# Optimization experiments

Measured on AMD Instinct MI355X. Metric: run time of the kernel, lower is better.

## Reference

```python
import jax, jax.numpy as jnp
import numpy as np


def _dwconv3x3(x, w, b):
    # depthwise 3x3, stride 1, padding 1 (groups == channels)
    y = jax.lax.conv_general_dilated(
        x, w, window_strides=(1, 1), padding=((1, 1), (1, 1)),
        dimension_numbers=('NCHW', 'OIHW', 'NCHW'),
        feature_group_count=x.shape[1])
    return y + b[None, :, None, None]


def _maxpool(x, f):
    # adaptive_max_pool2d to (h//f, w//f) with h,w divisible by f == stride-f max pool
    return jax.lax.reduce_window(x, -jnp.inf, jax.lax.max,
                                 (1, 1, f, f), (1, 1, f, f), 'VALID')


def _up_nearest(x, f):
    return jnp.repeat(jnp.repeat(x, f, axis=2), f, axis=3)


def setup_inputs() -> dict:
    key = jax.random.key(0)
    ks = jax.random.split(key, 10)
    B, C, H, W = 4, 32, 128, 128
    x = jax.random.normal(ks[0], (B, C, H, W), dtype=jnp.float32)
    mk = lambda k, shape, s: jax.random.normal(k, shape, dtype=jnp.float32) * s
    return {
        'x': x,
        'w0': mk(ks[1], (C, 1, 3, 3), 0.3), 'b0': mk(ks[2], (C,), 0.05),
        'w1': mk(ks[3], (C, 1, 3, 3), 0.3), 'b1': mk(ks[4], (C,), 0.05),
        'w2': mk(ks[5], (C, 1, 3, 3), 0.3), 'b2': mk(ks[6], (C,), 0.05),
        'wa': mk(ks[7], (C, C, 1, 1), 0.2), 'ba': mk(ks[8], (C,), 0.05),
    }


def reference(x, w0, b0, w1, b1, w2, b2, wa, ba):
    b, c, h, w = x.shape
    # multi-scale depthwise feature refinement
    s0 = _dwconv3x3(x, w0, b0)                               # level 0: full res
    s1 = _up_nearest(_dwconv3x3(_maxpool(x, 2), w1, b1), 2)  # level 1: /2
    s2 = _up_nearest(_dwconv3x3(_maxpool(x, 4), w2, b2), 4)  # level 2: /4
    # Channel_mixing8: q=s0, k=s1, v=s2; per-pixel CxC outer product
    to_nc = lambda t: t.transpose(0, 2, 3, 1).reshape(-1, c)  # (N, C), N=b*h*w
    q, k, v = to_nc(s0), to_nc(s1), to_nc(s2)
    kv = v[:, :, None] * k[:, None, :]        # (N, C, C) = v_embed @ k_embed^T
    attn = jax.nn.softmax(kv, axis=1)         # softmax over dim=1 (v axis)
    qkv = jnp.einsum('nij,nj->ni', attn, q)   # matvec with q
    out = qkv.reshape(b, h, w, c).transpose(0, 3, 1, 2)
    # aggr: 1x1 conv; drop_path=0 -> identity
    out = jnp.einsum('bchw,oc->bohw', out, wa[:, :, 0, 0]) + ba[None, :, None, None]
    return jax.nn.gelu(out, approximate=False) * x
```

## Files before the change

kernel.cpp:

```cpp
#include <hip/hip_runtime.h>
#include <hip/hip_fp16.h>
#include <math.h>


__device__ __forceinline__ float2 h2f2(unsigned int u) {
  __half2 h = *reinterpret_cast<__half2*>(&u);
  return __half22float2(h);
}
__device__ __forceinline__ unsigned int f2h2(float a, float b) {
  __half2 h = __floats2half2_rn(a, b);
  return *reinterpret_cast<unsigned int*>(&h);
}

__global__ __launch_bounds__(256) void fused_safm(
    const float* __restrict__ x,
    const float* __restrict__ w0, const float* __restrict__ b0,
    const float* __restrict__ w1, const float* __restrict__ b1,
    const float* __restrict__ w2, const float* __restrict__ b2,
    const float* __restrict__ wa, const float* __restrict__ ba,
    float* __restrict__ out) {
  int bid = blockIdx.x;
  int tw = bid & 7, th = (bid >> 3) & 63, b = bid >> 9;
  int t = threadIdx.x;
  int h4 = th >> 1;

  __shared__ __align__(16) unsigned int regA[4128];
  __shared__ __align__(16) float s0s[1056];
  __shared__ __align__(16) float vsh[288];
  __shared__ __align__(16) float qkvs[1056];
  __shared__ __align__(16) float rds[264];
  float* p1s = (float*)regA;

  {
#pragma unroll
    for (int kk = 0; kk < 9; ++kk) {
      int idx = t + kk * 256;
      int c = idx / 72, rem = idx % 72;
      int r = rem / 12, w = rem % 12;
      int pr = 2 * h4 - 2 + r, pc = 8 * tw - 2 + w;
      float v = 0.f;
      if ((unsigned)pr < 64u && (unsigned)pc < 64u) {
        const float* xp = x + ((size_t)(b * 32 + c) << 14) + 2 * pr * 128 + 2 * pc;
        float2 r0 = *(const float2*)xp;
        float2 r1 = *(const float2*)(xp + 128);
        v = fmaxf(fmaxf(r0.x, r0.y), fmaxf(r1.x, r1.y));
      }
      p1s[c * 73 + r * 12 + w] = v;
    }
  }
  {
    int c = t >> 3, gg = t & 7;
    int hh = gg >> 2, wb = (gg & 3) * 4;
    const float* xp = x + ((size_t)(b * 32 + c) << 14);
    const float* wc = w0 + c * 9;
    float wv[9];
#pragma unroll
    for (int q = 0; q < 9; ++q) wv[q] = wc[q];
    float bz = b0[c];
    float a0 = bz, a1 = bz, a2 = bz, a3 = bz;
    int cbase = 16 * tw + wb;
#pragma unroll
    for (int dr = -1; dr <= 1; ++dr) {
      int row = 2 * th + hh + dr;
      if ((unsigned)row >= 128u) continue;
      const float* rp = xp + row * 128 + cbase;
      float cm1 = (cbase > 0)       ? rp[-1] : 0.f;
      float4 c03 = *(const float4*)rp;
      float c4  = (cbase + 4 < 128) ? rp[4]  : 0.f;
      float wA = wv[(dr + 1) * 3], wB = wv[(dr + 1) * 3 + 1], wC = wv[(dr + 1) * 3 + 2];
      a0 = fmaf(wA, cm1,   fmaf(wB, c03.x, fmaf(wC, c03.y, a0)));
      a1 = fmaf(wA, c03.x, fmaf(wB, c03.y, fmaf(wC, c03.z, a1)));
      a2 = fmaf(wA, c03.y, fmaf(wB, c03.z, fmaf(wC, c03.w, a2)));
      a3 = fmaf(wA, c03.z, fmaf(wB, c03.w, fmaf(wC, c4,    a3)));
    }
    int pb = hh * 16 + wb;
    s0s[(pb)     * 33 + c] = a0;
    s0s[(pb + 1) * 33 + c] = a1;
    s0s[(pb + 2) * 33 + c] = a2;
    s0s[(pb + 3) * 33 + c] = a3;
  }
  __syncthreads();

  int ebT = t >> 5, jT = t & 31;
  float kreg;
  {
    const float* wc = w1 + jT * 9;
    const float* Pk = p1s + jT * 73 + ((th & 1) + 1) * 12 + ebT + 1;
    float acc = b1[jT];
    acc = fmaf(wc[0], Pk[0],  fmaf(wc[1], Pk[1],  fmaf(wc[2], Pk[2],  acc)));
    acc = fmaf(wc[3], Pk[12], fmaf(wc[4], Pk[13], fmaf(wc[5], Pk[14], acc)));
    acc = fmaf(wc[6], Pk[24], fmaf(wc[7], Pk[25], fmaf(wc[8], Pk[26], acc)));
    kreg = acc;
  }
  {
    const float* wc = w2 + jT * 9;
    const float* P = p1s + jT * 73;
    int cb0 = 2 * (ebT >> 1);
    float acc = b2[jT];
#pragma unroll
    for (int hq = 0; hq < 3; ++hq) {
      const float* Pr = P + 2 * hq * 12;
#pragma unroll
      for (int wq = 0; wq < 3; ++wq) {
        int cb = cb0 + 2 * wq;
        float p2v = fmaxf(fmaxf(Pr[cb], Pr[cb + 1]), fmaxf(Pr[cb + 12], Pr[cb + 13]));
        acc = fmaf(wc[hq * 3 + wq], p2v, acc);
      }
    }
    vsh[ebT * 36 + jT] = acc;
  }
  __syncthreads();

  {
    const float* vb = vsh + ebT * 36;
    const float4* v4 = (const float4*)vb;
    float4 q0 = v4[0];
    float vmax = fmaxf(fmaxf(q0.x, q0.y), fmaxf(q0.z, q0.w));
    float vmin = fminf(fminf(q0.x, q0.y), fminf(q0.z, q0.w));
#pragma unroll
    for (int iq = 1; iq < 8; ++iq) {
      float4 q_ = v4[iq];
      vmax = fmaxf(vmax, fmaxf(fmaxf(q_.x, q_.y), fmaxf(q_.z, q_.w)));
      vmin = fminf(vmin, fminf(fminf(q_.x, q_.y), fminf(q_.z, q_.w)));
    }
    const float L2E = 1.4426950408889634f;
    float m  = (kreg >= 0.f) ? kreg * vmax : kreg * vmin;
    float kl = kreg * L2E;
    float nm = -m * L2E;
    float d0 = 0.f, d1 = 0.f;
    unsigned int* EB = regA + ebT * 516 + jT;
#pragma unroll
    for (int ip = 0; ip < 16; ++ip) {
      float2 vp = *(const float2*)(vb + 2 * ip);
      float e0 = __builtin_amdgcn_exp2f(fmaf(vp.x, kl, nm));
      float e1 = __builtin_amdgcn_exp2f(fmaf(vp.y, kl, nm));
      d0 += e0; d1 += e1;
      EB[ip * 32] = f2h2(e0, e1);
    }
    rds[ebT * 33 + jT] = __fdividef(1.f, d0 + d1);
  }
  __syncthreads();

  {
    int p = t & 31, ic = t >> 5;
    int eb = (p & 15) >> 1;
    const unsigned int* EB = regA + eb * 516;
    const float* qrow = s0s + p * 33;
    const float* rdr = rds + eb * 33;
    float a0 = 0.f, a1 = 0.f, a2 = 0.f, a3 = 0.f;
#pragma unroll
    for (int jw = 0; jw < 8; ++jw) {
      uint4 wA = *(const uint4*)(EB + (2 * ic)     * 32 + jw * 4);
      uint4 wB = *(const uint4*)(EB + (2 * ic + 1) * 32 + jw * 4);
      float q0 = qrow[4 * jw]     * rdr[4 * jw];
      float q1 = qrow[4 * jw + 1] * rdr[4 * jw + 1];
      float q2 = qrow[4 * jw + 2] * rdr[4 * jw + 2];
      float q3 = qrow[4 * jw + 3] * rdr[4 * jw + 3];
      float2 f;
      f = h2f2(wA.x); a0 = fmaf(f.x, q0, a0); a1 = fmaf(f.y, q0, a1);
      f = h2f2(wA.y); a0 = fmaf(f.x, q1, a0); a1 = fmaf(f.y, q1, a1);
      f = h2f2(wA.z); a0 = fmaf(f.x, q2, a0); a1 = fmaf(f.y, q2, a1);
      f = h2f2(wA.w); a0 = fmaf(f.x, q3, a0); a1 = fmaf(f.y, q3, a1);
      f = h2f2(wB.x); a2 = fmaf(f.x, q0, a2); a3 = fmaf(f.y, q0, a3);
      f = h2f2(wB.y); a2 = fmaf(f.x, q1, a2); a3 = fmaf(f.y, q1, a3);
      f = h2f2(wB.z); a2 = fmaf(f.x, q2, a2); a3 = fmaf(f.y, q2, a3);
      f = h2f2(wB.w); a2 = fmaf(f.x, q3, a2); a3 = fmaf(f.y, q3, a3);
    }
    float* qd = qkvs + p * 33 + ic * 4;
    qd[0] = a0; qd[1] = a1; qd[2] = a2; qd[3] = a3;
  }
  __syncthreads();

  {
    int o = t >> 3, g = t & 7;
    int hh = g >> 2, wb = (g & 3) * 4;
    const float* wo = wa + o * 32;
    const float* q0 = qkvs + (hh * 16 + wb)     * 33;
    const float* q1 = qkvs + (hh * 16 + wb + 1) * 33;
    const float* q2 = qkvs + (hh * 16 + wb + 2) * 33;
    const float* q3 = qkvs + (hh * 16 + wb + 3) * 33;
    float bz = ba[o];
    float y0 = bz, y1 = bz, y2 = bz, y3 = bz;
#pragma unroll
    for (int i = 0; i < 32; ++i) {
      float w = wo[i];
      y0 = fmaf(w, q0[i], y0);
      y1 = fmaf(w, q1[i], y1);
      y2 = fmaf(w, q2[i], y2);
      y3 = fmaf(w, q3[i], y3);
    }
    const float RS2 = 0.70710678118654752f;
    float g0 = 0.5f * y0 * (1.f + erff(y0 * RS2));
    float g1 = 0.5f * y1 * (1.f + erff(y1 * RS2));
    float g2 = 0.5f * y2 * (1.f + erff(y2 * RS2));
    float g3 = 0.5f * y3 * (1.f + erff(y3 * RS2));
    size_t ob = (((size_t)(b * 32 + o) * 128) + (2 * th + hh)) * 128 + 16 * tw + wb;
    float4 xv = *(const float4*)(x + ob);
    float4 r;
    r.x = g0 * xv.x; r.y = g1 * xv.y; r.z = g2 * xv.z; r.w = g3 * xv.w;
    *(float4*)(out + ob) = r;
  }
}

extern "C" void kernel_launch(void* const* d_in, const int* in_sizes, int n_in,
                              void* d_out, int out_size, void* d_ws, size_t ws_size,
                              hipStream_t stream) {
  const float* x  = (const float*)d_in[0];
  const float* w0 = (const float*)d_in[1];
  const float* b0 = (const float*)d_in[2];
  const float* w1 = (const float*)d_in[3];
  const float* b1 = (const float*)d_in[4];
  const float* w2 = (const float*)d_in[5];
  const float* b2 = (const float*)d_in[6];
  const float* wa = (const float*)d_in[7];
  const float* ba = (const float*)d_in[8];
  float* out = (float*)d_out;

  fused_safm<<<2048, 256, 0, stream>>>(x, w0, b0, w1, b1, w2, b2, wa, ba, out);
}
```

Measured before the change: 106.6 us.

## Use packed fp16 dot2 for attention matvec and vectorize shared-memory layouts

The softmax exponentials are now stored transposed as individual halves, and q is pre-scaled by the reciprocal denominator and stored as fp16, so the matvec can run on v_dot2 fp16 instructions instead of convert-plus-FMA chains. The maxpool prologue loads float4 vectors covering four pooled columns per thread, the pooled tile's channel stride becomes 76 to allow vector stores, and the qkv buffer uses a swizzled layout that permits float4 reads in the 1x1 conv stage. This trades fewer instructions and LDS transactions for q being rounded to fp16 and for a larger shared-memory footprint, which may lower occupancy.

```diff
diff --git a/kernel.cpp b/kernel.cpp
--- a/kernel.cpp
+++ b/kernel.cpp
@@ -3,14 +3,16 @@
 #include <math.h>
 
 
-__device__ __forceinline__ float2 h2f2(unsigned int u) {
-  __half2 h = *reinterpret_cast<__half2*>(&u);
-  return __half22float2(h);
-}
-__device__ __forceinline__ unsigned int f2h2(float a, float b) {
-  __half2 h = __floats2half2_rn(a, b);
-  return *reinterpret_cast<unsigned int*>(&h);
-}
+typedef _Float16 half2_t __attribute__((ext_vector_type(2)));
+
+__device__ __forceinline__ half2_t bch2(unsigned int u) {
+  return __builtin_bit_cast(half2_t, u);
+}
+__device__ __forceinline__ float fdot2(unsigned int a, unsigned int b, float c) {
+  return __builtin_amdgcn_fdot2(bch2(a), bch2(b), c, false);
+}
+
+__device__ __forceinline__ int QS(int p) { return p * 64 + (((p >> 2) & 7) << 2); }
 
 __global__ __launch_bounds__(256) void fused_safm(
     const float* __restrict__ x,
@@ -25,27 +27,52 @@
   int h4 = th >> 1;
 
   __shared__ __align__(16) unsigned int regA[4128];
+  __shared__ __align__(16) unsigned int qrdsh[544];
   __shared__ __align__(16) float s0s[1056];
   __shared__ __align__(16) float vsh[288];
-  __shared__ __align__(16) float qkvs[1056];
-  __shared__ __align__(16) float rds[264];
+  __shared__ __align__(16) float qkvs[2048];
   float* p1s = (float*)regA;
 
   {
-#pragma unroll
-    for (int kk = 0; kk < 9; ++kk) {
-      int idx = t + kk * 256;
-      int c = idx / 72, rem = idx % 72;
-      int r = rem / 12, w = rem % 12;
-      int pr = 2 * h4 - 2 + r, pc = 8 * tw - 2 + w;
-      float v = 0.f;
-      if ((unsigned)pr < 64u && (unsigned)pc < 64u) {
-        const float* xp = x + ((size_t)(b * 32 + c) << 14) + 2 * pr * 128 + 2 * pc;
-        float2 r0 = *(const float2*)xp;
-        float2 r1 = *(const float2*)(xp + 128);
-        v = fmaxf(fmaxf(r0.x, r0.y), fmaxf(r1.x, r1.y));
+    const float* xb = x + ((size_t)(b * 32) << 14);
+#pragma unroll
+    for (int k = 0; k < 3; ++k) {
+      int idx = t + k * 256;
+      if (idx < 576) {
+        int c = idx / 18, rem = idx % 18;
+        int r = rem / 3, s = rem % 3;
+        int pr = 2 * h4 - 2 + r;
+        int pc0 = 8 * tw - 2 + 4 * s;
+        float m0 = 0.f, m1 = 0.f, m2 = 0.f, m3 = 0.f;
+        if ((unsigned)pr < 64u) {
+          const float* xp = xb + ((size_t)c << 14) + (2 * pr) * 128;
+          if (pc0 >= 0 && pc0 + 3 < 64) {
+            const float* q = xp + 2 * pc0;
+            float4 a0 = *(const float4*)q;
+            float4 a1 = *(const float4*)(q + 4);
+            float4 c0 = *(const float4*)(q + 128);
+            float4 c1 = *(const float4*)(q + 132);
+            m0 = fmaxf(fmaxf(a0.x, a0.y), fmaxf(c0.x, c0.y));
+            m1 = fmaxf(fmaxf(a0.z, a0.w), fmaxf(c0.z, c0.w));
+            m2 = fmaxf(fmaxf(a1.x, a1.y), fmaxf(c1.x, c1.y));
+            m3 = fmaxf(fmaxf(a1.z, a1.w), fmaxf(c1.z, c1.w));
+          } else {
+            float mm[4] = {0.f, 0.f, 0.f, 0.f};
+#pragma unroll
+            for (int m_ = 0; m_ < 4; ++m_) {
+              int pc = pc0 + m_;
+              if ((unsigned)pc < 64u) {
+                const float* q = xp + 2 * pc;
+                float2 r0 = *(const float2*)q;
+                float2 r1 = *(const float2*)(q + 128);
+                mm[m_] = fmaxf(fmaxf(r0.x, r0.y), fmaxf(r1.x, r1.y));
+              }
+            }
+            m0 = mm[0]; m1 = mm[1]; m2 = mm[2]; m3 = mm[3];
+          }
+        }
+        *(float4*)(p1s + c * 76 + r * 12 + 4 * s) = make_float4(m0, m1, m2, m3);
       }
-      p1s[c * 73 + r * 12 + w] = v;
     }
   }
   {
@@ -85,7 +112,7 @@
   float kreg;
   {
     const float* wc = w1 + jT * 9;
-    const float* Pk = p1s + jT * 73 + ((th & 1) + 1) * 12 + ebT + 1;
+    const float* Pk = p1s + jT * 76 + ((th & 1) + 1) * 12 + ebT + 1;
     float acc = b1[jT];
     acc = fmaf(wc[0], Pk[0],  fmaf(wc[1], Pk[1],  fmaf(wc[2], Pk[2],  acc)));
     acc = fmaf(wc[3], Pk[12], fmaf(wc[4], Pk[13], fmaf(wc[5], Pk[14], acc)));
@@ -94,16 +121,16 @@
   }
   {
     const float* wc = w2 + jT * 9;
-    const float* P = p1s + jT * 73;
-    int cb0 = 2 * (ebT >> 1);
+    const float* P = p1s + jT * 76 + 2 * (ebT >> 1);
     float acc = b2[jT];
 #pragma unroll
     for (int hq = 0; hq < 3; ++hq) {
       const float* Pr = P + 2 * hq * 12;
 #pragma unroll
       for (int wq = 0; wq < 3; ++wq) {
-        int cb = cb0 + 2 * wq;
-        float p2v = fmaxf(fmaxf(Pr[cb], Pr[cb + 1]), fmaxf(Pr[cb + 12], Pr[cb + 13]));
+        float2 u0 = *(const float2*)(Pr + 2 * wq);
+        float2 u1 = *(const float2*)(Pr + 2 * wq + 12);
+        float p2v = fmaxf(fmaxf(u0.x, u0.y), fmaxf(u1.x, u1.y));
         acc = fmaf(wc[hq * 3 + wq], p2v, acc);
       }
     }
@@ -128,46 +155,56 @@
     float kl = kreg * L2E;
     float nm = -m * L2E;
     float d0 = 0.f, d1 = 0.f;
-    unsigned int* EB = regA + ebT * 516 + jT;
+    __half* Eh = (__half*)regA;
+    int colbase = ebT * 1032 + jT;
 #pragma unroll
     for (int ip = 0; ip < 16; ++ip) {
       float2 vp = *(const float2*)(vb + 2 * ip);
       float e0 = __builtin_amdgcn_exp2f(fmaf(vp.x, kl, nm));
       float e1 = __builtin_amdgcn_exp2f(fmaf(vp.y, kl, nm));
       d0 += e0; d1 += e1;
-      EB[ip * 32] = f2h2(e0, e1);
-    }
-    rds[ebT * 33 + jT] = __fdividef(1.f, d0 + d1);
+      Eh[colbase + (2 * ip) * 32]     = __float2half(e0);
+      Eh[colbase + (2 * ip + 1) * 32] = __float2half(e1);
+    }
+    float rd = __fdividef(1.f, d0 + d1);
+    __half* Qh = (__half*)qrdsh;
+    int qbase = ebT * 136 + jT;
+#pragma unroll
+    for (int px = 0; px < 4; ++px) {
+      int hh = px >> 1, wwb = px & 1;
+      int p = hh * 16 + ebT * 2 + wwb;
+      float qv = s0s[p * 33 + jT] * rd;
+      Qh[qbase + px * 32] = __float2half(qv);
+    }
   }
   __syncthreads();
 
   {
     int p = t & 31, ic = t >> 5;
     int eb = (p & 15) >> 1;
-    const unsigned int* EB = regA + eb * 516;
-    const float* qrow = s0s + p * 33;
-    const float* rdr = rds + eb * 33;
-    float a0 = 0.f, a1 = 0.f, a2 = 0.f, a3 = 0.f;
-#pragma unroll
-    for (int jw = 0; jw < 8; ++jw) {
-      uint4 wA = *(const uint4*)(EB + (2 * ic)     * 32 + jw * 4);
-      uint4 wB = *(const uint4*)(EB + (2 * ic + 1) * 32 + jw * 4);
-      float q0 = qrow[4 * jw]     * rdr[4 * jw];
-      float q1 = qrow[4 * jw + 1] * rdr[4 * jw + 1];
-      float q2 = qrow[4 * jw + 2] * rdr[4 * jw + 2];
-      float q3 = qrow[4 * jw + 3] * rdr[4 * jw + 3];
-      float2 f;
-      f = h2f2(wA.x); a0 = fmaf(f.x, q0, a0); a1 = fmaf(f.y, q0, a1);
-      f = h2f2(wA.y); a0 = fmaf(f.x, q1, a0); a1 = fmaf(f.y, q1, a1);
-      f = h2f2(wA.z); a0 = fmaf(f.x, q2, a0); a1 = fmaf(f.y, q2, a1);
-      f = h2f2(wA.w); a0 = fmaf(f.x, q3, a0); a1 = fmaf(f.y, q3, a1);
-      f = h2f2(wB.x); a2 = fmaf(f.x, q0, a2); a3 = fmaf(f.y, q0, a3);
-      f = h2f2(wB.y); a2 = fmaf(f.x, q1, a2); a3 = fmaf(f.y, q1, a3);
-      f = h2f2(wB.z); a2 = fmaf(f.x, q2, a2); a3 = fmaf(f.y, q2, a3);
-      f = h2f2(wB.w); a2 = fmaf(f.x, q3, a2); a3 = fmaf(f.y, q3, a3);
-    }
-    float* qd = qkvs + p * 33 + ic * 4;
-    qd[0] = a0; qd[1] = a1; qd[2] = a2; qd[3] = a3;
+    int px = 2 * (p >> 4) + (p & 1);
+    const uint4* Eq = (const uint4*)(regA + eb * 516);
+    const uint4* Uq = (const uint4*)(qrdsh + eb * 68 + px * 16);
+    uint4 u0 = Uq[0], u1 = Uq[1], u2 = Uq[2], u3 = Uq[3];
+    float a0, a1, a2, a3;
+#define SAFM_ROW(di, dst)                                              \
+    {                                                                  \
+      const uint4* Er = Eq + (4 * ic + di) * 4;                        \
+      uint4 w0_ = Er[0], w1_ = Er[1], w2_ = Er[2], w3_ = Er[3];        \
+      float s_ = 0.f;                                                  \
+      s_ = fdot2(w0_.x, u0.x, s_); s_ = fdot2(w0_.y, u0.y, s_);        \
+      s_ = fdot2(w0_.z, u0.z, s_); s_ = fdot2(w0_.w, u0.w, s_);        \
+      s_ = fdot2(w1_.x, u1.x, s_); s_ = fdot2(w1_.y, u1.y, s_);        \
+      s_ = fdot2(w1_.z, u1.z, s_); s_ = fdot2(w1_.w, u1.w, s_);        \
+      s_ = fdot2(w2_.x, u2.x, s_); s_ = fdot2(w2_.y, u2.y, s_);        \
+      s_ = fdot2(w2_.z, u2.z, s_); s_ = fdot2(w2_.w, u2.w, s_);        \
+      s_ = fdot2(w3_.x, u3.x, s_); s_ = fdot2(w3_.y, u3.y, s_);        \
+      s_ = fdot2(w3_.z, u3.z, s_); s_ = fdot2(w3_.w, u3.w, s_);        \
+      dst = s_;                                                        \
+    }
+    SAFM_ROW(0, a0) SAFM_ROW(1, a1) SAFM_ROW(2, a2) SAFM_ROW(3, a3)
+#undef SAFM_ROW
+    *(float4*)(qkvs + QS(p) + 4 * ic) = make_float4(a0, a1, a2, a3);
   }
   __syncthreads();
 
@@ -175,19 +212,23 @@
     int o = t >> 3, g = t & 7;
     int hh = g >> 2, wb = (g & 3) * 4;
     const float* wo = wa + o * 32;
-    const float* q0 = qkvs + (hh * 16 + wb)     * 33;
-    const float* q1 = qkvs + (hh * 16 + wb + 1) * 33;
-    const float* q2 = qkvs + (hh * 16 + wb + 2) * 33;
-    const float* q3 = qkvs + (hh * 16 + wb + 3) * 33;
+    const float* qA = qkvs + QS(hh * 16 + wb);
+    const float* qB = qkvs + QS(hh * 16 + wb + 1);
+    const float* qC = qkvs + QS(hh * 16 + wb + 2);
+    const float* qD = qkvs + QS(hh * 16 + wb + 3);
     float bz = ba[o];
     float y0 = bz, y1 = bz, y2 = bz, y3 = bz;
 #pragma unroll
-    for (int i = 0; i < 32; ++i) {
-      float w = wo[i];
-      y0 = fmaf(w, q0[i], y0);
-      y1 = fmaf(w, q1[i], y1);
-      y2 = fmaf(w, q2[i], y2);
-      y3 = fmaf(w, q3[i], y3);
+    for (int m = 0; m < 8; ++m) {
+      float4 fA = *(const float4*)(qA + 4 * m);
+      float4 fB = *(const float4*)(qB + 4 * m);
+      float4 fC = *(const float4*)(qC + 4 * m);
+      float4 fD = *(const float4*)(qD + 4 * m);
+      float wv0 = wo[4 * m], wv1 = wo[4 * m + 1], wv2 = wo[4 * m + 2], wv3 = wo[4 * m + 3];
+      y0 = fmaf(wv0, fA.x, fmaf(wv1, fA.y, fmaf(wv2, fA.z, fmaf(wv3, fA.w, y0))));
+      y1 = fmaf(wv0, fB.x, fmaf(wv1, fB.y, fmaf(wv2, fB.z, fmaf(wv3, fB.w, y1))));
+      y2 = fmaf(wv0, fC.x, fmaf(wv1, fC.y, fmaf(wv2, fC.z, fmaf(wv3, fC.w, y2))));
+      y3 = fmaf(wv0, fD.x, fmaf(wv1, fD.y, fmaf(wv2, fD.z, fmaf(wv3, fD.w, y3))));
     }
     const float RS2 = 0.70710678118654752f;
     float g0 = 0.5f * y0 * (1.f + erff(y0 * RS2));
```

Measured after the change: 105.5 us. Within noise of the previous version (-1.0%).
